# Kernel tuning notes

Hardware: AMD Instinct MI355X
Metric: run time of the kernel (lower is better)

Reference implementation:

```python
import jax, jax.numpy as jnp
import numpy as np

DIST_THD = 2.0  # squared-distance threshold from my_chamfer_fn


def setup_inputs() -> dict:
    key = jax.random.key(0)
    k1, k2 = jax.random.split(key)
    pc1 = jax.random.normal(k1, (1, 16384, 3), dtype=jnp.float32)
    pc2 = jax.random.normal(k2, (1, 16384, 3), dtype=jnp.float32)
    return {"pc1": pc1, "pc2": pc2}


def _chamfer(x, y):
    # x: (N, P1, D), y: (N, P2, D). Squared pairwise distances (as pytorch3d knn_points).
    x2 = jnp.sum(x * x, axis=-1)                       # (N, P1)
    y2 = jnp.sum(y * y, axis=-1)                       # (N, P2)
    xy = jnp.einsum('npd,nqd->npq', x, y)              # (N, P1, P2)
    d2 = x2[:, :, None] + y2[:, None, :] - 2.0 * xy    # (N, P1, P2)
    cham_x = jnp.min(d2, axis=2)                       # (N, P1) NN dist x->y (K=1)
    cham_y = jnp.min(d2, axis=1)                       # (N, P2) NN dist y->x
    # threshold mask: distances >= 2 are zeroed
    cham_x = jnp.where(cham_x >= DIST_THD, 0.0, cham_x)
    cham_y = jnp.where(cham_y >= DIST_THD, 0.0, cham_y)
    N, P1, _ = x.shape
    P2 = y.shape[1]
    # point_reduction='mean' (lengths are full P), batch_reduction='mean'
    cx = jnp.sum(cham_x, axis=1) / P1
    cy = jnp.sum(cham_y, axis=1) / P2
    return jnp.sum(cx) / N + jnp.sum(cy) / N


def reference(pc1, pc2):
    # Chamfer loss between pc1 and pc2 (the kernel inside NSFP optimization);
    # normals are unused in this code path, so only the distance loss is returned.
    return _chamfer(pc1, pc2)
```

## Files before the change

kernel.cpp:

```cpp
#include <hip/hip_runtime.h>
#include <hip/hip_bf16.h>


constexpr int P      = 16384;
constexpr int BLK    = 256;
constexpr int NSEG   = 8;
constexpr int SEGPTS = P / NSEG;
constexpr int ROUND  = 1024;
constexpr int TILES  = ROUND / 32;
constexpr int ROWSB  = 256;

typedef short s8v  __attribute__((ext_vector_type(8)));
typedef float f16v __attribute__((ext_vector_type(16)));

static __device__ inline unsigned short bf16r(float f) {
    unsigned u = __float_as_uint(f);
    u = (u + 0x7FFFu + ((u >> 16) & 1u)) >> 16;
    return (unsigned short)u;
}
static __device__ inline float bf2f(unsigned short h) {
    return __uint_as_float(((unsigned)h) << 16);
}

static __device__ inline void encA(float a, float b, float c, unsigned e[8]) {
    const unsigned ONE = 0x3F80u;
    const float s = fmaf(a, a, fmaf(b, b, c * c));
    const unsigned short ah = bf16r(a), bh = bf16r(b), ch = bf16r(c);
    const unsigned short al = bf16r(a - bf2f(ah));
    const unsigned short bl = bf16r(b - bf2f(bh));
    const unsigned short cl = bf16r(c - bf2f(ch));
    const unsigned short sh = bf16r(s), sl = bf16r(s - bf2f(sh));
    e[0] = ah | ((unsigned)al << 16);
    e[1] = bh | ((unsigned)bl << 16);
    e[2] = ch | ((unsigned)cl << 16);
    e[3] = ah | ((unsigned)bh << 16);
    e[4] = ch | ((unsigned)sh << 16);
    e[5] = sl | (ONE << 16);
    e[6] = ONE;
    e[7] = 0;
}

static __device__ inline void encB(float a, float b, float c, unsigned e[8]) {
    const unsigned ONE = 0x3F80u;
    const float s = fmaf(a, a, fmaf(b, b, c * c));
    const unsigned short ah = bf16r(a), bh = bf16r(b), ch = bf16r(c);
    const unsigned short al = bf16r(a - bf2f(ah));
    const unsigned short bl = bf16r(b - bf2f(bh));
    const unsigned short cl = bf16r(c - bf2f(ch));
    const unsigned short sh = bf16r(s), sl = bf16r(s - bf2f(sh));
    const unsigned short Ah = bf16r(-2.f * bf2f(ah)), Bh = bf16r(-2.f * bf2f(bh));
    const unsigned short Ch = bf16r(-2.f * bf2f(ch));
    const unsigned short Al = bf16r(-2.f * bf2f(al)), Bl = bf16r(-2.f * bf2f(bl));
    const unsigned short Cl = bf16r(-2.f * bf2f(cl));
    e[0] = Ah | ((unsigned)Ah << 16);
    e[1] = Bh | ((unsigned)Bh << 16);
    e[2] = Ch | ((unsigned)Ch << 16);
    e[3] = Al | ((unsigned)Bl << 16);
    e[4] = Cl | (ONE << 16);
    e[5] = ONE | ((unsigned)sh << 16);
    e[6] = sl;
    e[7] = 0;
}

__global__ __launch_bounds__(BLK, 4) void chamfer_mfma(
    const float* __restrict__ pc1, const float* __restrict__ pc2,
    float* __restrict__ part,
    float* __restrict__ out)
{
    if (blockIdx.x == 0 && blockIdx.y == 0 && blockIdx.z == 0 && threadIdx.x == 0)
        out[0] = 0.0f;

    const int dir = blockIdx.z;
    const float* xs = dir ? pc2 : pc1;
    const float* ys = dir ? pc1 : pc2;

    __shared__ __align__(16) unsigned char ytile[ROUND * 32];

    const int tid  = threadIdx.x;
    const int lane = tid & 63;
    const int wv   = tid >> 6;
    const int l31  = lane & 31;
    const int half = lane >> 5;

    const int rowbase = blockIdx.x * ROWSB + wv * 64;
    s8v afrag[2];
    #pragma unroll
    for (int s = 0; s < 2; ++s) {
        const int p = rowbase + s * 32 + l31;
        unsigned e[8];
        encA(xs[3 * p], xs[3 * p + 1], xs[3 * p + 2], e);
        union { uint4 i; s8v v; } lo, hi;
        lo.i = make_uint4(e[0], e[1], e[2], e[3]);
        hi.i = make_uint4(e[4], e[5], e[6], e[7]);
        afrag[s] = half ? hi.v : lo.v;
    }

    f16v acc0, acc1, Z;
    #pragma unroll
    for (int i = 0; i < 16; ++i) { acc0[i] = 3.0e38f; acc1[i] = 3.0e38f; Z[i] = 0.0f; }

    const int segbase = blockIdx.y * SEGPTS;
    for (int r = 0; r < SEGPTS / ROUND; ++r) {
        #pragma unroll 2
        for (int j = 0; j < ROUND / BLK; ++j) {
            const int i = tid + j * BLK;
            const int q = segbase + r * ROUND + i;
            unsigned e[8];
            encB(ys[3 * q], ys[3 * q + 1], ys[3 * q + 2], e);
            const int tt = i >> 5, cc = i & 31;
            *(uint4*)(ytile + tt * 1024 +       cc * 16) = make_uint4(e[0], e[1], e[2], e[3]);
            *(uint4*)(ytile + tt * 1024 + 512 + cc * 16) = make_uint4(e[4], e[5], e[6], e[7]);
        }
        __syncthreads();

        const unsigned char* rp = ytile + lane * 16;
        #pragma unroll 2
        for (int t = 0; t < TILES; ++t) {
            const s8v bfrag = *(const s8v*)(rp + t * 1024);
            const f16v d0 = __builtin_amdgcn_mfma_f32_32x32x16_bf16(afrag[0], bfrag, Z, 0, 0, 0);
            acc0 = __builtin_elementwise_min(acc0, d0);
            const f16v d1 = __builtin_amdgcn_mfma_f32_32x32x16_bf16(afrag[1], bfrag, Z, 0, 0, 0);
            acc1 = __builtin_elementwise_min(acc1, d1);
        }
        __syncthreads();
    }

    float* pbase = part + ((size_t)(dir * NSEG + blockIdx.y)) * P;
    #pragma unroll
    for (int s = 0; s < 2; ++s) {
        #pragma unroll
        for (int rg = 0; rg < 16; ++rg) {
            float v = s ? acc1[rg] : acc0[rg];
            v = fminf(v, __shfl_xor(v, 1, 64));
            v = fminf(v, __shfl_xor(v, 2, 64));
            v = fminf(v, __shfl_xor(v, 4, 64));
            v = fminf(v, __shfl_xor(v, 8, 64));
            v = fminf(v, __shfl_xor(v, 16, 64));
            if (l31 == 0) {
                const int row = rowbase + s * 32 + (rg & 3) + 8 * (rg >> 2) + 4 * half;
                pbase[row] = v;
            }
        }
    }
}

__global__ __launch_bounds__(BLK) void chamfer_reduce(
    const float* __restrict__ part, float* __restrict__ out)
{
    const int gid = blockIdx.x * BLK + threadIdx.x;
    const int dirbase = (gid >= P) ? NSEG * P : 0;
    const int row = gid & (P - 1);

    float m = part[dirbase + row];
    #pragma unroll
    for (int s = 1; s < NSEG; ++s) m = fminf(m, part[dirbase + s * P + row]);

    if (m >= 2.0f) m = 0.0f;
    float v = m * (1.0f / (float)P);

    #pragma unroll
    for (int off = 32; off > 0; off >>= 1) v += __shfl_down(v, off, 64);

    __shared__ float wsum[BLK / 64];
    const int lane = threadIdx.x & 63;
    const int wvi = threadIdx.x >> 6;
    if (lane == 0) wsum[wvi] = v;
    __syncthreads();
    if (threadIdx.x == 0) {
        float ssum = wsum[0];
        #pragma unroll
        for (int w = 1; w < BLK / 64; ++w) ssum += wsum[w];
        atomicAdd(out, ssum);
    }
}

extern "C" void kernel_launch(void* const* d_in, const int* in_sizes, int n_in,
                              void* d_out, int out_size, void* d_ws, size_t ws_size,
                              hipStream_t stream) {
    const float* pc1 = (const float*)d_in[0];
    const float* pc2 = (const float*)d_in[1];
    float* out = (float*)d_out;
    float* part = (float*)d_ws;

    dim3 grid(P / ROWSB, NSEG, 2);
    chamfer_mfma<<<grid, BLK, 0, stream>>>(pc1, pc2, part, out);
    chamfer_reduce<<<(2 * P) / BLK, BLK, 0, stream>>>(part, out);
}
```

Before: 84.18 us.

## Compute both chamfer directions from one distance pass using atomic column minima

Drops the second grid direction that recomputed the transposed distance matrix. Each pc1×pc2 tile is now computed once: row minima stay in the MFMA accumulators, and column minima are found per tile with a cross-lane reduction and written with atomicMin on an order-preserving unsigned float encoding. This roughly halves MFMA and encoding work. In exchange it adds per-tile VALU reductions, many global atomics with contention across row blocks, and a memset launch to initialise the column buffer.

```diff
diff --git a/kernel.cpp b/kernel.cpp
--- a/kernel.cpp
+++ b/kernel.cpp
@@ -2,13 +2,14 @@
 #include <hip/hip_bf16.h>
 
 
-constexpr int P      = 16384;
-constexpr int BLK    = 256;
-constexpr int NSEG   = 8;
-constexpr int SEGPTS = P / NSEG;
-constexpr int ROUND  = 1024;
-constexpr int TILES  = ROUND / 32;
-constexpr int ROWSB  = 256;
+constexpr int P     = 16384;
+constexpr int BLK   = 256;
+constexpr int ROWSB = 256;
+constexpr int COLSB = 1024;
+constexpr int NROWG = P / ROWSB;
+constexpr int NCOLG = P / COLSB;
+constexpr int ROUND = 512;
+constexpr int TILES = ROUND / 32;
 
 typedef short s8v  __attribute__((ext_vector_type(8)));
 typedef float f16v __attribute__((ext_vector_type(16)));
@@ -20,6 +21,15 @@
 }
 static __device__ inline float bf2f(unsigned short h) {
     return __uint_as_float(((unsigned)h) << 16);
+}
+
+static __device__ inline unsigned enc_f32(float f) {
+    unsigned b = __float_as_uint(f);
+    return (b & 0x80000000u) ? ~b : (b | 0x80000000u);
+}
+static __device__ inline float dec_f32(unsigned u) {
+    unsigned b = (u & 0x80000000u) ? (u & 0x7FFFFFFFu) : ~u;
+    return __uint_as_float(b);
 }
 
 static __device__ inline void encA(float a, float b, float c, unsigned e[8]) {
@@ -64,15 +74,12 @@
 
 __global__ __launch_bounds__(BLK, 4) void chamfer_mfma(
     const float* __restrict__ pc1, const float* __restrict__ pc2,
-    float* __restrict__ part,
+    float* __restrict__ rowpart,
+    unsigned* __restrict__ colmin,
     float* __restrict__ out)
 {
-    if (blockIdx.x == 0 && blockIdx.y == 0 && blockIdx.z == 0 && threadIdx.x == 0)
+    if (blockIdx.x == 0 && blockIdx.y == 0 && threadIdx.x == 0)
         out[0] = 0.0f;
-
-    const int dir = blockIdx.z;
-    const float* xs = dir ? pc2 : pc1;
-    const float* ys = dir ? pc1 : pc2;
 
     __shared__ __align__(16) unsigned char ytile[ROUND * 32];
 
@@ -88,7 +95,7 @@
     for (int s = 0; s < 2; ++s) {
         const int p = rowbase + s * 32 + l31;
         unsigned e[8];
-        encA(xs[3 * p], xs[3 * p + 1], xs[3 * p + 2], e);
+        encA(pc1[3 * p], pc1[3 * p + 1], pc1[3 * p + 2], e);
         union { uint4 i; s8v v; } lo, hi;
         lo.i = make_uint4(e[0], e[1], e[2], e[3]);
         hi.i = make_uint4(e[4], e[5], e[6], e[7]);
@@ -99,14 +106,15 @@
     #pragma unroll
     for (int i = 0; i < 16; ++i) { acc0[i] = 3.0e38f; acc1[i] = 3.0e38f; Z[i] = 0.0f; }
 
-    const int segbase = blockIdx.y * SEGPTS;
-    for (int r = 0; r < SEGPTS / ROUND; ++r) {
-        #pragma unroll 2
+    const int colbase = blockIdx.y * COLSB;
+    for (int r = 0; r < COLSB / ROUND; ++r) {
+        __syncthreads();
+        #pragma unroll
         for (int j = 0; j < ROUND / BLK; ++j) {
             const int i = tid + j * BLK;
-            const int q = segbase + r * ROUND + i;
+            const int q = colbase + r * ROUND + i;
             unsigned e[8];
-            encB(ys[3 * q], ys[3 * q + 1], ys[3 * q + 2], e);
+            encB(pc2[3 * q], pc2[3 * q + 1], pc2[3 * q + 2], e);
             const int tt = i >> 5, cc = i & 31;
             *(uint4*)(ytile + tt * 1024 +       cc * 16) = make_uint4(e[0], e[1], e[2], e[3]);
             *(uint4*)(ytile + tt * 1024 + 512 + cc * 16) = make_uint4(e[4], e[5], e[6], e[7]);
@@ -118,14 +126,21 @@
         for (int t = 0; t < TILES; ++t) {
             const s8v bfrag = *(const s8v*)(rp + t * 1024);
             const f16v d0 = __builtin_amdgcn_mfma_f32_32x32x16_bf16(afrag[0], bfrag, Z, 0, 0, 0);
+            const f16v d1 = __builtin_amdgcn_mfma_f32_32x32x16_bf16(afrag[1], bfrag, Z, 0, 0, 0);
             acc0 = __builtin_elementwise_min(acc0, d0);
-            const f16v d1 = __builtin_amdgcn_mfma_f32_32x32x16_bf16(afrag[1], bfrag, Z, 0, 0, 0);
             acc1 = __builtin_elementwise_min(acc1, d1);
+            float m = fminf(d0[0], d0[1]);
+            #pragma unroll
+            for (int i = 2; i < 16; ++i) m = fminf(m, d0[i]);
+            #pragma unroll
+            for (int i = 0; i < 16; ++i) m = fminf(m, d1[i]);
+            m = fminf(m, __shfl_xor(m, 32, 64));
+            if (lane < 32)
+                atomicMin(&colmin[colbase + r * ROUND + t * 32 + l31], enc_f32(m));
         }
-        __syncthreads();
-    }
-
-    float* pbase = part + ((size_t)(dir * NSEG + blockIdx.y)) * P;
+    }
+
+    float* rowp = rowpart + (size_t)blockIdx.y * P;
     #pragma unroll
     for (int s = 0; s < 2; ++s) {
         #pragma unroll
@@ -138,22 +153,27 @@
             v = fminf(v, __shfl_xor(v, 16, 64));
             if (l31 == 0) {
                 const int row = rowbase + s * 32 + (rg & 3) + 8 * (rg >> 2) + 4 * half;
-                pbase[row] = v;
+                rowp[row] = v;
             }
         }
     }
 }
 
 __global__ __launch_bounds__(BLK) void chamfer_reduce(
-    const float* __restrict__ part, float* __restrict__ out)
+    const float* __restrict__ rowpart, const unsigned* __restrict__ colmin,
+    float* __restrict__ out)
 {
     const int gid = blockIdx.x * BLK + threadIdx.x;
-    const int dirbase = (gid >= P) ? NSEG * P : 0;
-    const int row = gid & (P - 1);
-
-    float m = part[dirbase + row];
-    #pragma unroll
-    for (int s = 1; s < NSEG; ++s) m = fminf(m, part[dirbase + s * P + row]);
+    const int p = gid & (P - 1);
+
+    float m;
+    if (gid < P) {
+        m = rowpart[p];
+        #pragma unroll
+        for (int s = 1; s < NCOLG; ++s) m = fminf(m, rowpart[(size_t)s * P + p]);
+    } else {
+        m = dec_f32(colmin[p]);
+    }
 
     if (m >= 2.0f) m = 0.0f;
     float v = m * (1.0f / (float)P);
@@ -180,9 +200,12 @@
     const float* pc1 = (const float*)d_in[0];
     const float* pc2 = (const float*)d_in[1];
     float* out = (float*)d_out;
-    float* part = (float*)d_ws;
-
-    dim3 grid(P / ROWSB, NSEG, 2);
-    chamfer_mfma<<<grid, BLK, 0, stream>>>(pc1, pc2, part, out);
-    chamfer_reduce<<<(2 * P) / BLK, BLK, 0, stream>>>(part, out);
-}
+    float* rowpart = (float*)d_ws;
+    unsigned* colmin = (unsigned*)(rowpart + (size_t)NCOLG * P);
+
+    hipMemsetAsync(colmin, 0xFF, (size_t)P * sizeof(unsigned), stream);
+
+    dim3 grid(NROWG, NCOLG);
+    chamfer_mfma<<<grid, BLK, 0, stream>>>(pc1, pc2, rowpart, colmin, out);
+    chamfer_reduce<<<(2 * P) / BLK, BLK, 0, stream>>>(rowpart, colmin, out);
+}
```

Result: slower. 91.24 us (+8.4%).
